# Kernel optimization log

Measured on AMD Instinct MI355X. Metric: run time of the kernel, lower is better.

Reference implementation:

```python
import jax, jax.numpy as jnp
import numpy as np

B, S, ENC = 64, 2048, 1024          # batch, encoder seq len, encoder feature dim
U, E_DIM, V_SZ = 512, 256, 50000    # dec_units, embedding_dim, vocab_size
IN_DIM = ENC + E_DIM                # LSTM input: [context ; token embedding]


def setup_inputs() -> dict:
    key = jax.random.key(0)
    ks = jax.random.split(key, 16)
    g = lambda k, shp, s=0.02: (jax.random.normal(k, shp, jnp.float32) * s)
    return {
        "x": jax.random.randint(ks[0], (B, 1), 0, V_SZ),
        "c_fwd": g(ks[1], (B, U), 0.1),
        "c_bwd": g(ks[2], (B, U), 0.1),
        "enc_output": jax.random.normal(ks[3], (B, S, ENC), jnp.float32),
        "emb": g(ks[4], (V_SZ, E_DIM)),
        "W1_w": g(ks[5], (ENC, U)), "W1_b": jnp.zeros((U,), jnp.float32),
        "W2_w": g(ks[6], (U, U)),   "W2_b": jnp.zeros((U,), jnp.float32),
        "W3_w": g(ks[7], (U, U)),   "W3_b": jnp.zeros((U,), jnp.float32),
        "V_w": g(ks[8], (U, 1)),    "V_b": jnp.zeros((1,), jnp.float32),
        "Kf": g(ks[9], (IN_DIM, 4 * U)),  "bf": jnp.zeros((4 * U,), jnp.float32),
        "Kb": g(ks[10], (IN_DIM, 4 * U)), "bb": jnp.zeros((4 * U,), jnp.float32),
        "fc_w": g(ks[11], (2 * U, V_SZ)), "fc_b": jnp.zeros((V_SZ,), jnp.float32),
    }


def _lstm_step_zero_state(xin, K, b):
    # Keras LSTM single step from zero (h0, c0): recurrent term vanishes.
    # Gate order in Keras kernel: i, f, c(g), o.
    z = xin @ K + b
    i, f, g, o = jnp.split(z, 4, axis=-1)
    i, o = jax.nn.sigmoid(i), jax.nn.sigmoid(o)  # f gate multiplies c0=0
    c = i * jnp.tanh(g)
    h = o * jnp.tanh(c)
    return h, c


def reference(x, c_fwd, c_bwd, enc_output, emb,
              W1_w, W1_b, W2_w, W2_b, W3_w, W3_b, V_w, V_b,
              Kf, bf, Kb, bb, fc_w, fc_b):
    # Bahdanau additive attention: score [B, S, 1]
    hidden_proj = (c_fwd @ W2_w + W2_b + c_bwd @ W3_w + W3_b)[:, None, :]  # [B,1,U]
    score = jnp.tanh(enc_output @ W1_w + W1_b + hidden_proj) @ V_w + V_b
    attn = jax.nn.softmax(score, axis=1)                 # softmax over S
    ctx = jnp.sum(attn * enc_output, axis=1)             # [B, ENC]

    xe = emb[x[:, 0]]                                    # [B, E_DIM]
    xin = jnp.concatenate([ctx, xe], axis=-1)            # [B, ENC+E_DIM]

    # Bidirectional LSTM over a length-1 sequence from zero initial state:
    # both directions see the same single timestep with separate weights.
    hf, cf = _lstm_step_zero_state(xin, Kf, bf)
    hb, cb = _lstm_step_zero_state(xin, Kb, bb)

    out = jnp.concatenate([hf, hb], axis=-1)             # [B, 2U]
    logits = out @ fc_w + fc_b                           # [B, vocab]
    return logits, hf, cf, hb, cb
```

## Files before the change

kernel.cpp:

```cpp
#include <hip/hip_runtime.h>

using u16 = unsigned short;
typedef float f32x4 __attribute__((ext_vector_type(4)));
typedef __bf16 bf16x8 __attribute__((ext_vector_type(8)));
typedef u16 u16x8 __attribute__((ext_vector_type(8)));
typedef u16 u16x4 __attribute__((ext_vector_type(4)));

static constexpr int OF_HPB   = 262144;
static constexpr int OF_CTXP  = 294912;
static constexpr int OF_STATS = 2392064;
static constexpr int OF_XIN   = 2394112;
static constexpr int OF_ZPART = 2476032;
static constexpr size_t SCRATCH_FLOATS = 3000320;
static constexpr size_t SCRATCH_BYTES = SCRATCH_FLOATS * 4ull;

__device__ __forceinline__ u16 f2bf(float f) {
  unsigned u = __float_as_uint(f);
  u += 0x7FFFu + ((u >> 16) & 1u);
  return (u16)(u >> 16);
}
__device__ __forceinline__ float fast_tanh(float x) {
  x = fminf(fmaxf(x, -20.f), 20.f);
  float e = __expf(2.f * x);
  return (e - 1.f) / (e + 1.f);
}
__device__ __forceinline__ float fast_sig(float x) { return 1.f / (1.f + __expf(-x)); }

__device__ __forceinline__ void gll16(const u16* g, u16* l) {
  __builtin_amdgcn_global_load_lds(
      (const __attribute__((address_space(1))) unsigned int*)g,
      (__attribute__((address_space(3))) unsigned int*)l, 16, 0, 0);
}

__global__ void k_prep_w1(const float* __restrict__ W1w, u16* __restrict__ w1p) {
  __shared__ float tile[32][132];
  const int t = threadIdx.x;
  const int ks = blockIdx.x >> 2, u0 = (blockIdx.x & 3) * 128;
  {
    int kk = t >> 3, ui = (t & 7) * 16;
    const float* src = W1w + (size_t)(ks * 32 + kk) * 512 + u0 + ui;
    #pragma unroll
    for (int i = 0; i < 4; ++i)
      *(float4*)&tile[kk][ui + i * 4] = *(const float4*)(src + i * 4);
  }
  __syncthreads();
  {
    int u = t >> 1, kh = (t & 1) * 16;
    u16x8 p0, p1;
    #pragma unroll
    for (int i = 0; i < 8; ++i) {
      p0[i] = f2bf(tile[kh + i][u]);
      p1[i] = f2bf(tile[kh + 8 + i][u]);
    }
    u16* dst = w1p + ((size_t)ks * 512 + u0 + u) * 32 + kh;
    *(u16x8*)(dst)     = p0;
    *(u16x8*)(dst + 8) = p1;
  }
}

__global__ void k_prep_hp(const float* __restrict__ cf, const float* __restrict__ cb,
                          const float* __restrict__ W2w, const float* __restrict__ W2b,
                          const float* __restrict__ W3w, const float* __restrict__ W3b,
                          const float* __restrict__ W1b, float* __restrict__ hpb) {
  __shared__ float cfl[512], cbl[512];
  const int b = blockIdx.x, t = threadIdx.x;
  cfl[t] = cf[(size_t)b * 512 + t];       cfl[t + 256] = cf[(size_t)b * 512 + t + 256];
  cbl[t] = cb[(size_t)b * 512 + t];       cbl[t + 256] = cb[(size_t)b * 512 + t + 256];
  __syncthreads();
  const int u1 = t, u2 = t + 256;
  float a1 = W2b[u1] + W3b[u1] + W1b[u1];
  float a2 = W2b[u2] + W3b[u2] + W1b[u2];
  for (int k = 0; k < 512; ++k) {
    float c1 = cfl[k], c2 = cbl[k];
    const float* r2 = W2w + (size_t)k * 512;
    const float* r3 = W3w + (size_t)k * 512;
    a1 += c1 * r2[u1] + c2 * r3[u1];
    a2 += c1 * r2[u2] + c2 * r3[u2];
  }
  hpb[(size_t)b * 512 + u1] = a1;
  hpb[(size_t)b * 512 + u2] = a2;
}

__global__ void __launch_bounds__(512, 4)
k_attn(const float* __restrict__ enc, const u16* __restrict__ w1p,
       const float* __restrict__ hpb, const float* __restrict__ Vw,
       const float* __restrict__ Vb, float* __restrict__ ctxp,
       float* __restrict__ stats) {
  __shared__ __align__(16) u16 smem[40960];

  const int t = threadIdx.x;
  const int bid = blockIdx.x;
  const int b = bid >> 5, tile = bid & 31;
  const size_t row0 = (size_t)b * 2048 + (size_t)tile * 64;

  const int l = t & 63, w = t >> 6;
  const int ln = l & 15, lg = l >> 4;

  const int s_lg = (t >> 1) & 3, s_ln = (t >> 3) & 15, s_im = t >> 7, s_h = t & 1;
  const float* a_src = enc + (row0 + s_im * 16 + s_ln) * 1024 + s_lg * 8 + s_h * 4;

  f32x4 acc[4][4];
  #pragma unroll
  for (int im = 0; im < 4; ++im)
    #pragma unroll
    for (int nf = 0; nf < 4; ++nf)
      acc[im][nf] = f32x4{0.f, 0.f, 0.f, 0.f};

  {
    u16* Bn = smem;
    #pragma unroll
    for (int i = 0; i < 4; ++i)
      gll16(w1p + i * 4096 + t * 8, Bn + i * 4096 + w * 512);
    float4 av = *(const float4*)(a_src);
    u16x4 aw4;
    aw4[0] = f2bf(av.x); aw4[1] = f2bf(av.y); aw4[2] = f2bf(av.z); aw4[3] = f2bf(av.w);
    *(u16x4*)(smem + 32768 + t * 4) = aw4;
  }
  __syncthreads();

  for (int ks = 0; ks < 32; ++ks) {
    const int cur = ks & 1;
    u16* Bc = smem + cur * 16384;
    u16* Ac = smem + 32768 + cur * 4096;
    float4 av;
    if (ks < 31) {
      u16* Bn = smem + (cur ^ 1) * 16384;
      const u16* bsrc = w1p + (size_t)(ks + 1) * 16384 + t * 8;
      #pragma unroll
      for (int i = 0; i < 4; ++i)
        gll16(bsrc + i * 4096, Bn + i * 4096 + w * 512);
      av = *(const float4*)(a_src + (ks + 1) * 32);
    }
    bf16x8 afr[4], bfr[4];
    #pragma unroll
    for (int im = 0; im < 4; ++im)
      afr[im] = *(const bf16x8*)(Ac + im * 512 + ln * 32 + lg * 8);
    #pragma unroll
    for (int nf = 0; nf < 4; ++nf)
      bfr[nf] = *(const bf16x8*)(Bc + (w * 64 + nf * 16 + ln) * 32 + lg * 8);
    #pragma unroll
    for (int im = 0; im < 4; ++im)
      #pragma unroll
      for (int nf = 0; nf < 4; ++nf)
        acc[im][nf] = __builtin_amdgcn_mfma_f32_16x16x32_bf16(afr[im], bfr[nf], acc[im][nf], 0, 0, 0);
    if (ks < 31) {
      u16* An = smem + 32768 + (cur ^ 1) * 4096;
      u16x4 aw4;
      aw4[0] = f2bf(av.x); aw4[1] = f2bf(av.y); aw4[2] = f2bf(av.z); aw4[3] = f2bf(av.w);
      *(u16x4*)(An + t * 4) = aw4;
    }
    __syncthreads();
  }

  float* fsm = (float*)smem;
  float* red = fsm;
  float* scv = fsm + 576;
  float* pcv = fsm + 640;

  float vw_l[4], hp_l[4];
  #pragma unroll
  for (int nf = 0; nf < 4; ++nf) {
    int col = w * 64 + nf * 16 + ln;
    vw_l[nf] = Vw[col];
    hp_l[nf] = hpb[(size_t)b * 512 + col];
  }
  #pragma unroll
  for (int im = 0; im < 4; ++im) {
    #pragma unroll
    for (int r = 0; r < 4; ++r) {
      float s = 0.f;
      #pragma unroll
      for (int nf = 0; nf < 4; ++nf)
        s += vw_l[nf] * fast_tanh(acc[im][nf][r] + hp_l[nf]);
      s += __shfl_xor(s, 1);
      s += __shfl_xor(s, 2);
      s += __shfl_xor(s, 4);
      s += __shfl_xor(s, 8);
      if (ln == 0) red[(im * 16 + lg * 4 + r) * 9 + w] = s;
    }
  }
  __syncthreads();
  if (t < 64) {
    float s = Vb[0];
    #pragma unroll
    for (int w2 = 0; w2 < 8; ++w2) s += red[t * 9 + w2];
    float e = __expf(s);
    scv[t] = e;
    float p = e;
    p += __shfl_xor(p, 1);  p += __shfl_xor(p, 2);  p += __shfl_xor(p, 4);
    p += __shfl_xor(p, 8);  p += __shfl_xor(p, 16); p += __shfl_xor(p, 32);
    if (t == 0) stats[bid] = p;
  }
  __syncthreads();

  {
    const int c4 = (t & 255) * 4;
    const int rh = t >> 8;
    const float* ep = enc + (row0 + rh * 32) * 1024 + c4;
    float ax = 0.f, ay = 0.f, az = 0.f, aw2 = 0.f;
    #pragma unroll 4
    for (int r = 0; r < 32; ++r) {
      float4 v = *(const float4*)(ep + (size_t)r * 1024);
      float s = scv[rh * 32 + r];
      ax += s * v.x; ay += s * v.y; az += s * v.z; aw2 += s * v.w;
    }
    if (t >= 256) {
      float4 st = {ax, ay, az, aw2};
      *(float4*)&pcv[c4] = st;
    }
    __syncthreads();
    if (t < 256) {
      float4 p2 = *(const float4*)&pcv[c4];
      float4 o = {ax + p2.x, ay + p2.y, az + p2.z, aw2 + p2.w};
      *(float4*)&ctxp[(size_t)bid * 1024 + c4] = o;
    }
  }
}

__global__ void k_attn_reduce(const float* __restrict__ ctxp, const float* __restrict__ stats,
                              const int* __restrict__ x, const float* __restrict__ emb,
                              float* __restrict__ xin) {
  __shared__ float ps[32];
  __shared__ float invs;
  const int b = blockIdx.x, t = threadIdx.x;
  if (t < 32) ps[t] = stats[b * 32 + t];
  __syncthreads();
  if (t == 0) {
    float s = 0.f;
    #pragma unroll
    for (int i = 0; i < 32; ++i) s += ps[i];
    invs = 1.f / s;
  }
  __syncthreads();
  const float inv = invs;
  #pragma unroll
  for (int i = 0; i < 4; ++i) {
    int c = t + i * 256;
    float a = 0.f;
    for (int chv = 0; chv < 32; ++chv)
      a += ctxp[((size_t)b * 32 + chv) * 1024 + c];
    xin[(size_t)b * 1280 + c] = a * inv;
  }
  xin[(size_t)b * 1280 + 1024 + t] = emb[(size_t)x[b] * 256 + t];
}

__global__ void k_lstm_gemm(const float* __restrict__ xin, const float* __restrict__ Kf,
                            const float* __restrict__ Kb, float* __restrict__ zpart) {
  __shared__ float xl[32][68];
  const int t = threadIdx.x;
  const int bid = blockIdx.x;
  const int dir = bid >> 7;
  const int jt  = (bid >> 1) & 63;
  const int ks  = bid & 1;
  const float* K = dir ? Kb : Kf;
  const int j  = jt * 32 + (t & 31);
  const int tb = t >> 5;
  const int brow = t >> 2, kq = (t & 3) * 8;
  float acc[8] = {0,0,0,0,0,0,0,0};
  for (int k0 = ks * 640; k0 < ks * 640 + 640; k0 += 32) {
    float4 x0 = *(const float4*)&xin[(size_t)brow * 1280 + k0 + kq];
    float4 x1 = *(const float4*)&xin[(size_t)brow * 1280 + k0 + kq + 4];
    __syncthreads();
    xl[kq+0][brow]=x0.x; xl[kq+1][brow]=x0.y; xl[kq+2][brow]=x0.z; xl[kq+3][brow]=x0.w;
    xl[kq+4][brow]=x1.x; xl[kq+5][brow]=x1.y; xl[kq+6][brow]=x1.z; xl[kq+7][brow]=x1.w;
    __syncthreads();
    const float* Kp = K + (size_t)k0 * 2048 + j;
    #pragma unroll 8
    for (int kk = 0; kk < 32; ++kk) {
      float wv = Kp[(size_t)kk * 2048];
      float4 v0 = *(const float4*)&xl[kk][tb * 8];
      float4 v1 = *(const float4*)&xl[kk][tb * 8 + 4];
      acc[0] += v0.x * wv; acc[1] += v0.y * wv; acc[2] += v0.z * wv; acc[3] += v0.w * wv;
      acc[4] += v1.x * wv; acc[5] += v1.y * wv; acc[6] += v1.z * wv; acc[7] += v1.w * wv;
    }
  }
  float* zp = zpart + ((size_t)dir * 2 + ks) * 64 * 2048;
  #pragma unroll
  for (int i = 0; i < 8; ++i)
    zp[(size_t)(tb * 8 + i) * 2048 + j] = acc[i];
}

__global__ void k_gates(const float* __restrict__ zpart, const float* __restrict__ bfv,
                        const float* __restrict__ bbv, float* __restrict__ dout) {
  const int dir = blockIdx.x >> 6, b = blockIdx.x & 63, u = threadIdx.x;
  const float* bias = dir ? bbv : bfv;
  const float* z0 = zpart + ((size_t)dir * 2 + 0) * 131072 + (size_t)b * 2048;
  const float* z1 = zpart + ((size_t)dir * 2 + 1) * 131072 + (size_t)b * 2048;
  float zi = z0[u]        + z1[u]        + bias[u];
  float zg = z0[1024 + u] + z1[1024 + u] + bias[1024 + u];
  float zo = z0[1536 + u] + z1[1536 + u] + bias[1536 + u];
  float c = fast_sig(zi) * fast_tanh(zg);
  float h = fast_sig(zo) * fast_tanh(c);
  size_t base = 3200000u + (size_t)dir * 65536u;
  dout[base + (size_t)b * 512 + u] = h;
  dout[base + 32768u + (size_t)b * 512 + u] = c;
}

__global__ void __launch_bounds__(256)
k_fc(const float* __restrict__ dout_ro, const float* __restrict__ fcw,
     const float* __restrict__ fcb, float* __restrict__ logits) {
  __shared__ float ol[64][68];
  __shared__ float wl[64][132];
  const int t = threadIdx.x;
  const int j0 = blockIdx.x * 128;
  const int tb = t >> 5, tj = t & 31;
  const float* hf = dout_ro + 3200000u;
  const float* hb = dout_ro + 3200000u + 65536u;
  float acc[8][4];
  #pragma unroll
  for (int bi = 0; bi < 8; ++bi)
    #pragma unroll
    for (int ji = 0; ji < 4; ++ji) acc[bi][ji] = 0.f;

  for (int k0 = 0; k0 < 1024; k0 += 64) {
    __syncthreads();
    {
      int bb = t >> 2, kq = (t & 3) * 16;
      const float* src = (k0 < 512) ? (hf + (size_t)bb * 512 + k0 + kq)
                                    : (hb + (size_t)bb * 512 + (k0 - 512) + kq);
      #pragma unroll
      for (int i = 0; i < 4; ++i) {
        float4 v = *(const float4*)(src + i * 4);
        ol[kq + i*4 + 0][bb] = v.x;
        ol[kq + i*4 + 1][bb] = v.y;
        ol[kq + i*4 + 2][bb] = v.z;
        ol[kq + i*4 + 3][bb] = v.w;
      }
    }
    {
      int kk = t >> 2, jh = (t & 3) * 32;
      const float* wsrc = fcw + (size_t)(k0 + kk) * 50000 + j0 + jh;
      #pragma unroll
      for (int i = 0; i < 8; ++i) {
        int j = j0 + jh + i * 4;
        float4 v;
        if (j + 3 < 50000) {
          v = *(const float4*)(wsrc + i * 4);
        } else {
          v.x = (j + 0 < 50000) ? wsrc[i*4 + 0] : 0.f;
          v.y = (j + 1 < 50000) ? wsrc[i*4 + 1] : 0.f;
          v.z = (j + 2 < 50000) ? wsrc[i*4 + 2] : 0.f;
          v.w = 0.f;
        }
        *(float4*)&wl[kk][jh + i * 4] = v;
      }
    }
    __syncthreads();
    #pragma unroll 4
    for (int kk = 0; kk < 64; ++kk) {
      float4 wv = *(const float4*)&wl[kk][tj * 4];
      float4 q0 = *(const float4*)&ol[kk][tb * 8];
      float4 q1 = *(const float4*)&ol[kk][tb * 8 + 4];
      float obv[8] = {q0.x, q0.y, q0.z, q0.w, q1.x, q1.y, q1.z, q1.w};
      #pragma unroll
      for (int bi = 0; bi < 8; ++bi) {
        acc[bi][0] += obv[bi] * wv.x;
        acc[bi][1] += obv[bi] * wv.y;
        acc[bi][2] += obv[bi] * wv.z;
        acc[bi][3] += obv[bi] * wv.w;
      }
    }
  }

  const int j = j0 + tj * 4;
  if (j + 3 < 50000) {
    float4 fb = *(const float4*)(fcb + j);
    #pragma unroll
    for (int bi = 0; bi < 8; ++bi) {
      float4 r;
      r.x = acc[bi][0] + fb.x; r.y = acc[bi][1] + fb.y;
      r.z = acc[bi][2] + fb.z; r.w = acc[bi][3] + fb.w;
      *(float4*)&logits[(size_t)(tb * 8 + bi) * 50000 + j] = r;
    }
  } else {
    for (int ji = 0; ji < 4; ++ji) {
      if (j + ji < 50000) {
        float fb = fcb[j + ji];
        for (int bi = 0; bi < 8; ++bi)
          logits[(size_t)(tb * 8 + bi) * 50000 + j + ji] = acc[bi][ji] + fb;
      }
    }
  }
}

extern "C" void kernel_launch(void* const* d_in, const int* in_sizes, int n_in,
                              void* d_out, int out_size, void* d_ws, size_t ws_size,
                              hipStream_t stream) {
  const int*   x    = (const int*)  d_in[0];
  const float* cfwd = (const float*)d_in[1];
  const float* cbwd = (const float*)d_in[2];
  const float* enc  = (const float*)d_in[3];
  const float* emb  = (const float*)d_in[4];
  const float* W1w  = (const float*)d_in[5];
  const float* W1b  = (const float*)d_in[6];
  const float* W2w  = (const float*)d_in[7];
  const float* W2b  = (const float*)d_in[8];
  const float* W3w  = (const float*)d_in[9];
  const float* W3b  = (const float*)d_in[10];
  const float* Vw   = (const float*)d_in[11];
  const float* Vb   = (const float*)d_in[12];
  const float* Kf   = (const float*)d_in[13];
  const float* bfv  = (const float*)d_in[14];
  const float* Kb   = (const float*)d_in[15];
  const float* bbv  = (const float*)d_in[16];
  const float* fcw  = (const float*)d_in[17];
  const float* fcb  = (const float*)d_in[18];
  float* out = (float*)d_out;

  float* S = (ws_size >= SCRATCH_BYTES) ? (float*)d_ws : out;
  u16*   w1p   = (u16*)S;
  float* hpb   = S + OF_HPB;
  float* ctxp  = S + OF_CTXP;
  float* stats = S + OF_STATS;
  float* xin   = S + OF_XIN;
  float* zpart = S + OF_ZPART;

  k_prep_w1<<<128, 256, 0, stream>>>(W1w, w1p);
  k_prep_hp<<<64, 256, 0, stream>>>(cfwd, cbwd, W2w, W2b, W3w, W3b, W1b, hpb);
  k_attn<<<2048, 512, 0, stream>>>(enc, w1p, hpb, Vw, Vb, ctxp, stats);
  k_attn_reduce<<<64, 256, 0, stream>>>(ctxp, stats, x, emb, xin);
  k_lstm_gemm<<<256, 256, 0, stream>>>(xin, Kf, Kb, zpart);
  k_gates<<<128, 512, 0, stream>>>(zpart, bfv, bbv, out);
  k_fc<<<391, 256, 0, stream>>>(out, fcw, fcb, out);
}
```

Baseline: 541.6 us.

## Use bf16 MFMA for vocab projection and deepen attention GEMM prefetch pipeline

Adds a per-call pre-pass that converts fc_w to bf16 in a K-blocked layout, plus an MFMA-based vocab projection that splits the activations into bf16 hi and lo parts to keep fp32-like accuracy. This replaces the fp32 SIMT GEMM whenever the workspace is large enough. The attention GEMM gets a 3-deep register prefetch of encoder rows, relaid LDS fragments, explicit vmcnt waits with raw barriers, and setprio around the MFMA block, all to hide global load latency. The fc weight conversion reads the 200MB fp32 matrix and writes 100MB of bf16 on every call, which may cost more than the faster GEMM saves. The new path also depends on the workspace size.

```diff
diff --git a/kernel.cpp b/kernel.cpp
--- a/kernel.cpp
+++ b/kernel.cpp
@@ -12,12 +12,23 @@
 static constexpr int OF_XIN   = 2394112;
 static constexpr int OF_ZPART = 2476032;
 static constexpr size_t SCRATCH_FLOATS = 3000320;
-static constexpr size_t SCRATCH_BYTES = SCRATCH_FLOATS * 4ull;
+static constexpr size_t SCRATCH_BYTES  = SCRATCH_FLOATS * 4ull;
+static constexpr size_t OF_W2P_F       = 3000320;
+static constexpr size_t W2P_U16        = 50176ull * 1024ull;
+static constexpr size_t TOTAL_BYTES    = OF_W2P_F * 4ull + W2P_U16 * 2ull;
+
+#define FENCE()  asm volatile("" ::: "memory")
+#define VMCNT6() asm volatile("s_waitcnt vmcnt(6)" ::: "memory")
+#define VMCNT0() asm volatile("s_waitcnt vmcnt(0)" ::: "memory")
+#define LGKM0()  asm volatile("s_waitcnt lgkmcnt(0)" ::: "memory")
 
 __device__ __forceinline__ u16 f2bf(float f) {
   unsigned u = __float_as_uint(f);
   u += 0x7FFFu + ((u >> 16) & 1u);
   return (u16)(u >> 16);
+}
+__device__ __forceinline__ float bf2f(u16 u) {
+  return __uint_as_float((unsigned)u << 16);
 }
 __device__ __forceinline__ float fast_tanh(float x) {
   x = fminf(fmaxf(x, -20.f), 20.f);
@@ -81,12 +92,49 @@
   hpb[(size_t)b * 512 + u2] = a2;
 }
 
+__global__ void __launch_bounds__(256)
+k_prep_fcw(const float* __restrict__ fcw, u16* __restrict__ w2p) {
+  __shared__ float tl[32][260];
+  const int t = threadIdx.x;
+  const int jt = blockIdx.x >> 5, kt = blockIdx.x & 31;
+  const int j0 = jt * 256, k0 = kt * 32;
+  {
+    const int kk = t >> 3, c0 = (t & 7) * 32;
+    const float* src = fcw + (size_t)(k0 + kk) * 50000 + j0 + c0;
+    #pragma unroll
+    for (int i = 0; i < 8; ++i) {
+      int j = j0 + c0 + i * 4;
+      float4 v;
+      if (j + 3 < 50000) {
+        v = *(const float4*)(src + i * 4);
+      } else {
+        v.x = (j + 0 < 50000) ? src[i * 4 + 0] : 0.f;
+        v.y = (j + 1 < 50000) ? src[i * 4 + 1] : 0.f;
+        v.z = (j + 2 < 50000) ? src[i * 4 + 2] : 0.f;
+        v.w = 0.f;
+      }
+      *(float4*)&tl[kk][c0 + i * 4] = v;
+    }
+  }
+  __syncthreads();
+  {
+    u16* dst = w2p + ((size_t)kt * 50176 + j0 + t) * 32;
+    #pragma unroll
+    for (int q = 0; q < 4; ++q) {
+      u16x8 p;
+      #pragma unroll
+      for (int m = 0; m < 8; ++m) p[m] = f2bf(tl[q * 8 + m][t]);
+      *(u16x8*)(dst + q * 8) = p;
+    }
+  }
+}
+
 __global__ void __launch_bounds__(512, 4)
 k_attn(const float* __restrict__ enc, const u16* __restrict__ w1p,
        const float* __restrict__ hpb, const float* __restrict__ Vw,
        const float* __restrict__ Vb, float* __restrict__ ctxp,
        float* __restrict__ stats) {
-  __shared__ __align__(16) u16 smem[40960];
+  __shared__ __align__(16) u16 smem[36864];
 
   const int t = threadIdx.x;
   const int bid = blockIdx.x;
@@ -96,60 +144,107 @@
   const int l = t & 63, w = t >> 6;
   const int ln = l & 15, lg = l >> 4;
 
-  const int s_lg = (t >> 1) & 3, s_ln = (t >> 3) & 15, s_im = t >> 7, s_h = t & 1;
+  const int s_im = t >> 7, s_ln = (t >> 3) & 15, s_lg = (t >> 1) & 3, s_h = t & 1;
   const float* a_src = enc + (row0 + s_im * 16 + s_ln) * 1024 + s_lg * 8 + s_h * 4;
+  const int a_dst = (s_im * 64 + s_lg * 16 + s_ln) * 8 + s_h * 4;
+  const u16* bsrc = w1p + (size_t)(w * 64 + ln) * 32 + lg * 8;
+  u16* bdst = smem + w * 2048;
 
   f32x4 acc[4][4];
   #pragma unroll
   for (int im = 0; im < 4; ++im)
     #pragma unroll
-    for (int nf = 0; nf < 4; ++nf)
-      acc[im][nf] = f32x4{0.f, 0.f, 0.f, 0.f};
-
+    for (int nf = 0; nf < 4; ++nf) acc[im][nf] = f32x4{0.f, 0.f, 0.f, 0.f};
+
+  float4 avH0, avH1, avH2;
   {
-    u16* Bn = smem;
-    #pragma unroll
-    for (int i = 0; i < 4; ++i)
-      gll16(w1p + i * 4096 + t * 8, Bn + i * 4096 + w * 512);
-    float4 av = *(const float4*)(a_src);
-    u16x4 aw4;
-    aw4[0] = f2bf(av.x); aw4[1] = f2bf(av.y); aw4[2] = f2bf(av.z); aw4[3] = f2bf(av.w);
-    *(u16x4*)(smem + 32768 + t * 4) = aw4;
-  }
-  __syncthreads();
-
-  for (int ks = 0; ks < 32; ++ks) {
+    float4 av0 = *(const float4*)(a_src);
+    u16x4 aw;
+    aw[0]=f2bf(av0.x); aw[1]=f2bf(av0.y); aw[2]=f2bf(av0.z); aw[3]=f2bf(av0.w);
+    *(u16x4*)(smem + 32768 + a_dst) = aw;
+    FENCE();
+    avH0 = *(const float4*)(a_src + 32);
+    avH1 = *(const float4*)(a_src + 64);
+    FENCE();
+    gll16(bsrc,        bdst);
+    gll16(bsrc +  512, bdst +  512);
+    gll16(bsrc + 1024, bdst + 1024);
+    gll16(bsrc + 1536, bdst + 1536);
+    FENCE();
+    avH2 = *(const float4*)(a_src + 96);
+    FENCE();
+    LGKM0();
+    __builtin_amdgcn_s_barrier();
+  }
+
+  #pragma unroll 4
+  for (int ks = 0; ks < 28; ++ks) {
     const int cur = ks & 1;
-    u16* Bc = smem + cur * 16384;
-    u16* Ac = smem + 32768 + cur * 4096;
-    float4 av;
+    {
+      u16* bd = bdst + ((cur ^ 1) << 14);
+      const u16* bs = bsrc + (size_t)(ks + 1) * 16384;
+      gll16(bs, bd);               gll16(bs +  512, bd +  512);
+      gll16(bs + 1024, bd + 1024); gll16(bs + 1536, bd + 1536);
+    }
+    FENCE();
+    float4 avIn = *(const float4*)(a_src + (ks + 4) * 32);
+    FENCE();
+    VMCNT6();
+    const u16* Ac = smem + 32768 + (cur << 11);
+    const u16* Bc = smem + (cur << 14) + w * 2048;
+    bf16x8 afr[4], bfr[4];
+    #pragma unroll
+    for (int im = 0; im < 4; ++im) afr[im] = *(const bf16x8*)(Ac + im * 512 + l * 8);
+    #pragma unroll
+    for (int nf = 0; nf < 4; ++nf) bfr[nf] = *(const bf16x8*)(Bc + nf * 512 + l * 8);
+    __builtin_amdgcn_s_setprio(1);
+    #pragma unroll
+    for (int im = 0; im < 4; ++im)
+      #pragma unroll
+      for (int nf = 0; nf < 4; ++nf)
+        acc[im][nf] = __builtin_amdgcn_mfma_f32_16x16x32_bf16(afr[im], bfr[nf], acc[im][nf], 0, 0, 0);
+    __builtin_amdgcn_s_setprio(0);
+    {
+      u16* An = smem + 32768 + ((cur ^ 1) << 11);
+      u16x4 aw;
+      aw[0]=f2bf(avH0.x); aw[1]=f2bf(avH0.y); aw[2]=f2bf(avH0.z); aw[3]=f2bf(avH0.w);
+      *(u16x4*)(An + a_dst) = aw;
+    }
+    avH0 = avH1; avH1 = avH2; avH2 = avIn;
+    LGKM0();
+    __builtin_amdgcn_s_barrier();
+  }
+
+  for (int ks = 28; ks < 32; ++ks) {
+    const int cur = ks & 1;
     if (ks < 31) {
-      u16* Bn = smem + (cur ^ 1) * 16384;
-      const u16* bsrc = w1p + (size_t)(ks + 1) * 16384 + t * 8;
-      #pragma unroll
-      for (int i = 0; i < 4; ++i)
-        gll16(bsrc + i * 4096, Bn + i * 4096 + w * 512);
-      av = *(const float4*)(a_src + (ks + 1) * 32);
-    }
+      u16* bd = bdst + ((cur ^ 1) << 14);
+      const u16* bs = bsrc + (size_t)(ks + 1) * 16384;
+      gll16(bs, bd);               gll16(bs +  512, bd +  512);
+      gll16(bs + 1024, bd + 1024); gll16(bs + 1536, bd + 1536);
+    }
+    VMCNT0();
+    const u16* Ac = smem + 32768 + (cur << 11);
+    const u16* Bc = smem + (cur << 14) + w * 2048;
     bf16x8 afr[4], bfr[4];
     #pragma unroll
-    for (int im = 0; im < 4; ++im)
-      afr[im] = *(const bf16x8*)(Ac + im * 512 + ln * 32 + lg * 8);
-    #pragma unroll
-    for (int nf = 0; nf < 4; ++nf)
-      bfr[nf] = *(const bf16x8*)(Bc + (w * 64 + nf * 16 + ln) * 32 + lg * 8);
+    for (int im = 0; im < 4; ++im) afr[im] = *(const bf16x8*)(Ac + im * 512 + l * 8);
+    #pragma unroll
+    for (int nf = 0; nf < 4; ++nf) bfr[nf] = *(const bf16x8*)(Bc + nf * 512 + l * 8);
     #pragma unroll
     for (int im = 0; im < 4; ++im)
       #pragma unroll
       for (int nf = 0; nf < 4; ++nf)
         acc[im][nf] = __builtin_amdgcn_mfma_f32_16x16x32_bf16(afr[im], bfr[nf], acc[im][nf], 0, 0, 0);
     if (ks < 31) {
-      u16* An = smem + 32768 + (cur ^ 1) * 4096;
-      u16x4 aw4;
-      aw4[0] = f2bf(av.x); aw4[1] = f2bf(av.y); aw4[2] = f2bf(av.z); aw4[3] = f2bf(av.w);
-      *(u16x4*)(An + t * 4) = aw4;
-    }
-    __syncthreads();
+      u16* An = smem + 32768 + ((cur ^ 1) << 11);
+      u16x4 aw;
+      aw[0]=f2bf(avH0.x); aw[1]=f2bf(avH0.y); aw[2]=f2bf(avH0.z); aw[3]=f2bf(avH0.w);
+      *(u16x4*)(An + a_dst) = aw;
+      avH0 = avH1; avH1 = avH2;
+    }
+    LGKM0();
+    __builtin_amdgcn_s_barrier();
   }
 
   float* fsm = (float*)smem;
@@ -297,8 +392,117 @@
 }
 
 __global__ void __launch_bounds__(256)
-k_fc(const float* __restrict__ dout_ro, const float* __restrict__ fcw,
-     const float* __restrict__ fcb, float* __restrict__ logits) {
+k_fc_mfma(const float* __restrict__ hbase, const u16* __restrict__ w2p,
+          const float* __restrict__ fcb, float* __restrict__ logits) {
+  __shared__ __align__(16) u16 smem[24576];
+  const int t = threadIdx.x;
+  const int j0 = blockIdx.x * 256;
+  const int l = t & 63, w = t >> 6;
+  const int ln = l & 15, lg = l >> 4;
+
+  const int s_im = t >> 6, s_ln = (t >> 2) & 15, s_lg = t & 3;
+  const int a_chunk = (s_im * 64 + s_lg * 16 + s_ln) * 8;
+  const int a_row = s_im * 16 + s_ln;
+
+  const u16* bsrc = w2p + (size_t)(j0 + w * 64 + ln) * 32 + lg * 8;
+  u16* bdst = smem + w * 2048;
+
+  f32x4 acc[4][4];
+  #pragma unroll
+  for (int im = 0; im < 4; ++im)
+    #pragma unroll
+    for (int nf = 0; nf < 4; ++nf) acc[im][nf] = f32x4{0.f, 0.f, 0.f, 0.f};
+
+  {
+    gll16(bsrc,        bdst);
+    gll16(bsrc +  512, bdst +  512);
+    gll16(bsrc + 1024, bdst + 1024);
+    gll16(bsrc + 1536, bdst + 1536);
+    const float* hs = hbase + (size_t)a_row * 512 + s_lg * 8;
+    float4 v0 = *(const float4*)(hs);
+    float4 v1 = *(const float4*)(hs + 4);
+    float vv[8] = {v0.x, v0.y, v0.z, v0.w, v1.x, v1.y, v1.z, v1.w};
+    u16x8 hi, lo;
+    #pragma unroll
+    for (int jq = 0; jq < 8; ++jq) {
+      u16 h = f2bf(vv[jq]);
+      hi[jq] = h;
+      lo[jq] = f2bf(vv[jq] - bf2f(h));
+    }
+    *(u16x8*)(smem + 16384 + a_chunk) = hi;
+    *(u16x8*)(smem + 16384 + 2048 + a_chunk) = lo;
+  }
+  __syncthreads();
+
+  for (int ks = 0; ks < 32; ++ks) {
+    const int cur = ks & 1;
+    if (ks < 31) {
+      u16* bd = bdst + ((cur ^ 1) << 13);
+      const u16* bs = bsrc + (size_t)(ks + 1) * 1605632;
+      gll16(bs, bd);               gll16(bs +  512, bd +  512);
+      gll16(bs + 1024, bd + 1024); gll16(bs + 1536, bd + 1536);
+    }
+    const u16* Ac = smem + 16384 + (cur << 12);
+    const u16* Bc = smem + (cur << 13) + w * 2048;
+    bf16x8 ahi[4], alo[4], bfr[4];
+    #pragma unroll
+    for (int im = 0; im < 4; ++im) {
+      ahi[im] = *(const bf16x8*)(Ac + im * 512 + l * 8);
+      alo[im] = *(const bf16x8*)(Ac + 2048 + im * 512 + l * 8);
+    }
+    #pragma unroll
+    for (int nf = 0; nf < 4; ++nf) bfr[nf] = *(const bf16x8*)(Bc + nf * 512 + l * 8);
+    #pragma unroll
+    for (int im = 0; im < 4; ++im)
+      #pragma unroll
+      for (int nf = 0; nf < 4; ++nf) {
+        acc[im][nf] = __builtin_amdgcn_mfma_f32_16x16x32_bf16(alo[im], bfr[nf], acc[im][nf], 0, 0, 0);
+        acc[im][nf] = __builtin_amdgcn_mfma_f32_16x16x32_bf16(ahi[im], bfr[nf], acc[im][nf], 0, 0, 0);
+      }
+    if (ks < 31) {
+      const int kn = ks + 1;
+      const float* hs = hbase + (kn >= 16 ? 65536 : 0) + (size_t)a_row * 512 + (kn & 15) * 32 + s_lg * 8;
+      float4 v0 = *(const float4*)(hs);
+      float4 v1 = *(const float4*)(hs + 4);
+      float vv[8] = {v0.x, v0.y, v0.z, v0.w, v1.x, v1.y, v1.z, v1.w};
+      u16x8 hi, lo;
+      #pragma unroll
+      for (int jq = 0; jq < 8; ++jq) {
+        u16 h = f2bf(vv[jq]);
+        hi[jq] = h;
+        lo[jq] = f2bf(vv[jq] - bf2f(h));
+      }
+      u16* An = smem + 16384 + ((cur ^ 1) << 12);
+      *(u16x8*)(An + a_chunk) = hi;
+      *(u16x8*)(An + 2048 + a_chunk) = lo;
+    }
+    __syncthreads();
+  }
+
+  float fb[4];
+  #pragma unroll
+  for (int nf = 0; nf < 4; ++nf) {
+    int c = j0 + w * 64 + nf * 16 + ln;
+    fb[nf] = (c < 50000) ? fcb[c] : 0.f;
+  }
+  #pragma unroll
+  for (int im = 0; im < 4; ++im)
+    #pragma unroll
+    for (int nf = 0; nf < 4; ++nf) {
+      int c = j0 + w * 64 + nf * 16 + ln;
+      if (c < 50000) {
+        #pragma unroll
+        for (int r = 0; r < 4; ++r) {
+          int row = im * 16 + lg * 4 + r;
+          logits[(size_t)row * 50000 + c] = acc[im][nf][r] + fb[nf];
+        }
+      }
+    }
+}
+
+__global__ void __launch_bounds__(256)
+k_fc_f32(const float* __restrict__ dout_ro, const float* __restrict__ fcw,
+         const float* __restrict__ fcb, float* __restrict__ logits) {
   __shared__ float ol[64][68];
   __shared__ float wl[64][132];
   const int t = threadIdx.x;
@@ -407,19 +611,24 @@
   const float* fcb  = (const float*)d_in[18];
   float* out = (float*)d_out;
 
-  float* S = (ws_size >= SCRATCH_BYTES) ? (float*)d_ws : out;
+  const bool haveWs  = (ws_size >= SCRATCH_BYTES);
+  const bool bigWs   = (ws_size >= TOTAL_BYTES);
+  float* S = haveWs ? (float*)d_ws : out;
   u16*   w1p   = (u16*)S;
   float* hpb   = S + OF_HPB;
   float* ctxp  = S + OF_CTXP;
   float* stats = S + OF_STATS;
   float* xin   = S + OF_XIN;
   float* zpart = S + OF_ZPART;
+  u16*   w2p   = (u16*)(S + OF_W2P_F);
 
   k_prep_w1<<<128, 256, 0, stream>>>(W1w, w1p);
   k_prep_hp<<<64, 256, 0, stream>>>(cfwd, cbwd, W2w, W2b, W3w, W3b, W1b, hpb);
+  if (bigWs) k_prep_fcw<<<6272, 256, 0, stream>>>(fcw, w2p);
   k_attn<<<2048, 512, 0, stream>>>(enc, w1p, hpb, Vw, Vb, ctxp, stats);
   k_attn_reduce<<<64, 256, 0, stream>>>(ctxp, stats, x, emb, xin);
   k_lstm_gemm<<<256, 256, 0, stream>>>(xin, Kf, Kb, zpart);
   k_gates<<<128, 512, 0, stream>>>(zpart, bfv, bbv, out);
-  k_fc<<<391, 256, 0, stream>>>(out, fcw, fcb, out);
-}
+  if (bigWs) k_fc_mfma<<<196, 256, 0, stream>>>(out + 3200000u, w2p, fcb, out);
+  else       k_fc_f32<<<391, 256, 0, stream>>>(out, fcw, fcb, out);
+}
```

Result: slower. 591.1 us (+9.1%).

## Move vocab projection to bf16 MFMA with split-precision activations and relayout attention LDS

Applied to the files above, without the earlier changes.

The final FC GEMM (64x1024 by 1024x50000) moves from a scalar fp32 kernel to an MFMA kernel. Hidden states are split into bf16 hi/lo parts by the gates kernel, and fc weights are rounded to bf16 on the fly from a double-buffered LDS tile. The attention GEMM also changes its LDS layout so fragments are read contiguously, uses a smaller shared buffer, and prefetches the encoder rows one step further ahead. The trade-off is reduced weight precision, since the weights go to bf16 while only the activations keep hi/lo compensation, plus a fallback path when the workspace is too small.

```diff
diff --git a/kernel.cpp b/kernel.cpp
--- a/kernel.cpp
+++ b/kernel.cpp
@@ -11,13 +11,17 @@
 static constexpr int OF_STATS = 2392064;
 static constexpr int OF_XIN   = 2394112;
 static constexpr int OF_ZPART = 2476032;
-static constexpr size_t SCRATCH_FLOATS = 3000320;
-static constexpr size_t SCRATCH_BYTES = SCRATCH_FLOATS * 4ull;
+static constexpr int OF_HHL   = 3000320;
+static constexpr size_t SCRATCH_FLOATS = 3065856;
+static constexpr size_t SCRATCH_BYTES  = SCRATCH_FLOATS * 4ull;
 
 __device__ __forceinline__ u16 f2bf(float f) {
   unsigned u = __float_as_uint(f);
   u += 0x7FFFu + ((u >> 16) & 1u);
   return (u16)(u >> 16);
+}
+__device__ __forceinline__ float bf2f(u16 u) {
+  return __uint_as_float((unsigned)u << 16);
 }
 __device__ __forceinline__ float fast_tanh(float x) {
   x = fminf(fmaxf(x, -20.f), 20.f);
@@ -86,7 +90,7 @@
        const float* __restrict__ hpb, const float* __restrict__ Vw,
        const float* __restrict__ Vb, float* __restrict__ ctxp,
        float* __restrict__ stats) {
-  __shared__ __align__(16) u16 smem[40960];
+  __shared__ __align__(16) u16 smem[36864];
 
   const int t = threadIdx.x;
   const int bid = blockIdx.x;
@@ -96,59 +100,57 @@
   const int l = t & 63, w = t >> 6;
   const int ln = l & 15, lg = l >> 4;
 
-  const int s_lg = (t >> 1) & 3, s_ln = (t >> 3) & 15, s_im = t >> 7, s_h = t & 1;
+  const int s_im = t >> 7, s_ln = (t >> 3) & 15, s_lg = (t >> 1) & 3, s_h = t & 1;
   const float* a_src = enc + (row0 + s_im * 16 + s_ln) * 1024 + s_lg * 8 + s_h * 4;
+  const int a_dst = (s_im * 64 + s_lg * 16 + s_ln) * 8 + s_h * 4;
+  const u16* bsrc = w1p + (size_t)(w * 64 + ln) * 32 + lg * 8;
+  u16* bdst = smem + w * 2048;
 
   f32x4 acc[4][4];
   #pragma unroll
   for (int im = 0; im < 4; ++im)
     #pragma unroll
-    for (int nf = 0; nf < 4; ++nf)
-      acc[im][nf] = f32x4{0.f, 0.f, 0.f, 0.f};
-
+    for (int nf = 0; nf < 4; ++nf) acc[im][nf] = f32x4{0.f, 0.f, 0.f, 0.f};
+
+  float4 avB;
   {
-    u16* Bn = smem;
-    #pragma unroll
-    for (int i = 0; i < 4; ++i)
-      gll16(w1p + i * 4096 + t * 8, Bn + i * 4096 + w * 512);
-    float4 av = *(const float4*)(a_src);
-    u16x4 aw4;
-    aw4[0] = f2bf(av.x); aw4[1] = f2bf(av.y); aw4[2] = f2bf(av.z); aw4[3] = f2bf(av.w);
-    *(u16x4*)(smem + 32768 + t * 4) = aw4;
+    float4 av0 = *(const float4*)(a_src);
+    u16x4 aw;
+    aw[0]=f2bf(av0.x); aw[1]=f2bf(av0.y); aw[2]=f2bf(av0.z); aw[3]=f2bf(av0.w);
+    *(u16x4*)(smem + 32768 + a_dst) = aw;
+    gll16(bsrc,        bdst);
+    gll16(bsrc +  512, bdst +  512);
+    gll16(bsrc + 1024, bdst + 1024);
+    gll16(bsrc + 1536, bdst + 1536);
+    avB = *(const float4*)(a_src + 32);
   }
   __syncthreads();
 
   for (int ks = 0; ks < 32; ++ks) {
     const int cur = ks & 1;
-    u16* Bc = smem + cur * 16384;
-    u16* Ac = smem + 32768 + cur * 4096;
-    float4 av;
     if (ks < 31) {
-      u16* Bn = smem + (cur ^ 1) * 16384;
-      const u16* bsrc = w1p + (size_t)(ks + 1) * 16384 + t * 8;
-      #pragma unroll
-      for (int i = 0; i < 4; ++i)
-        gll16(bsrc + i * 4096, Bn + i * 4096 + w * 512);
-      av = *(const float4*)(a_src + (ks + 1) * 32);
-    }
+      u16* An = smem + 32768 + ((cur ^ 1) << 11);
+      u16x4 aw;
+      aw[0]=f2bf(avB.x); aw[1]=f2bf(avB.y); aw[2]=f2bf(avB.z); aw[3]=f2bf(avB.w);
+      *(u16x4*)(An + a_dst) = aw;
+      if (ks < 30) avB = *(const float4*)(a_src + (ks + 2) * 32);
+      u16* bd = bdst + ((cur ^ 1) << 14);
+      const u16* bs = bsrc + (size_t)(ks + 1) * 16384;
+      gll16(bs, bd);               gll16(bs +  512, bd +  512);
+      gll16(bs + 1024, bd + 1024); gll16(bs + 1536, bd + 1536);
+    }
+    const u16* Ac = smem + 32768 + (cur << 11);
+    const u16* Bc = smem + (cur << 14) + w * 2048;
     bf16x8 afr[4], bfr[4];
     #pragma unroll
-    for (int im = 0; im < 4; ++im)
-      afr[im] = *(const bf16x8*)(Ac + im * 512 + ln * 32 + lg * 8);
-    #pragma unroll
-    for (int nf = 0; nf < 4; ++nf)
-      bfr[nf] = *(const bf16x8*)(Bc + (w * 64 + nf * 16 + ln) * 32 + lg * 8);
+    for (int im = 0; im < 4; ++im) afr[im] = *(const bf16x8*)(Ac + im * 512 + l * 8);
+    #pragma unroll
+    for (int nf = 0; nf < 4; ++nf) bfr[nf] = *(const bf16x8*)(Bc + nf * 512 + l * 8);
     #pragma unroll
     for (int im = 0; im < 4; ++im)
       #pragma unroll
       for (int nf = 0; nf < 4; ++nf)
         acc[im][nf] = __builtin_amdgcn_mfma_f32_16x16x32_bf16(afr[im], bfr[nf], acc[im][nf], 0, 0, 0);
-    if (ks < 31) {
-      u16* An = smem + 32768 + (cur ^ 1) * 4096;
-      u16x4 aw4;
-      aw4[0] = f2bf(av.x); aw4[1] = f2bf(av.y); aw4[2] = f2bf(av.z); aw4[3] = f2bf(av.w);
-      *(u16x4*)(An + t * 4) = aw4;
-    }
     __syncthreads();
   }
 
@@ -281,7 +283,8 @@
 }
 
 __global__ void k_gates(const float* __restrict__ zpart, const float* __restrict__ bfv,
-                        const float* __restrict__ bbv, float* __restrict__ dout) {
+                        const float* __restrict__ bbv, float* __restrict__ dout,
+                        u16* __restrict__ hhl) {
   const int dir = blockIdx.x >> 6, b = blockIdx.x & 63, u = threadIdx.x;
   const float* bias = dir ? bbv : bfv;
   const float* z0 = zpart + ((size_t)dir * 2 + 0) * 131072 + (size_t)b * 2048;
@@ -294,11 +297,119 @@
   size_t base = 3200000u + (size_t)dir * 65536u;
   dout[base + (size_t)b * 512 + u] = h;
   dout[base + 32768u + (size_t)b * 512 + u] = c;
+  u16 hi = f2bf(h);
+  u16 lo = f2bf(h - bf2f(hi));
+  hhl[(size_t)b * 1024 + dir * 512 + u] = hi;
+  hhl[65536u + (size_t)b * 1024 + dir * 512 + u] = lo;
 }
 
 __global__ void __launch_bounds__(256)
-k_fc(const float* __restrict__ dout_ro, const float* __restrict__ fcw,
-     const float* __restrict__ fcb, float* __restrict__ logits) {
+k_fc_mfma(const float* __restrict__ fcw, const u16* __restrict__ hhl,
+          const float* __restrict__ fcb, float* __restrict__ logits) {
+  __shared__ float Bs[2][32 * 136];
+  const int t = threadIdx.x;
+  const int j0 = blockIdx.x * 128;
+  const int l = t & 63, w = t >> 6;
+  const int ln = l & 15, lg = l >> 4;
+  const int srow = t >> 3, scol = (t & 7) * 16;
+  const bool interior = (j0 + 128 <= 50000);
+
+  f32x4 acc[4][2];
+  #pragma unroll
+  for (int im = 0; im < 4; ++im)
+    #pragma unroll
+    for (int nf = 0; nf < 2; ++nf) acc[im][nf] = f32x4{0.f, 0.f, 0.f, 0.f};
+
+  float4 pre[4];
+  {
+    const float* src = fcw + (size_t)srow * 50000 + j0 + scol;
+    if (interior) {
+      #pragma unroll
+      for (int q = 0; q < 4; ++q) pre[q] = *(const float4*)(src + q * 4);
+    } else {
+      #pragma unroll
+      for (int q = 0; q < 4; ++q) {
+        int jb = j0 + scol + q * 4;
+        pre[q].x = (jb + 0 < 50000) ? src[q*4 + 0] : 0.f;
+        pre[q].y = (jb + 1 < 50000) ? src[q*4 + 1] : 0.f;
+        pre[q].z = (jb + 2 < 50000) ? src[q*4 + 2] : 0.f;
+        pre[q].w = (jb + 3 < 50000) ? src[q*4 + 3] : 0.f;
+      }
+    }
+    #pragma unroll
+    for (int q = 0; q < 4; ++q)
+      *(float4*)&Bs[0][srow * 136 + scol + q * 4] = pre[q];
+  }
+  __syncthreads();
+
+  for (int ks = 0; ks < 32; ++ks) {
+    const int cur = ks & 1;
+    if (ks < 31) {
+      const float* src = fcw + (size_t)(ks + 1) * 32 * 50000 + (size_t)srow * 50000 + j0 + scol;
+      if (interior) {
+        #pragma unroll
+        for (int q = 0; q < 4; ++q) pre[q] = *(const float4*)(src + q * 4);
+      } else {
+        #pragma unroll
+        for (int q = 0; q < 4; ++q) {
+          int jb = j0 + scol + q * 4;
+          pre[q].x = (jb + 0 < 50000) ? src[q*4 + 0] : 0.f;
+          pre[q].y = (jb + 1 < 50000) ? src[q*4 + 1] : 0.f;
+          pre[q].z = (jb + 2 < 50000) ? src[q*4 + 2] : 0.f;
+          pre[q].w = (jb + 3 < 50000) ? src[q*4 + 3] : 0.f;
+        }
+      }
+    }
+    bf16x8 ahi[4], alo[4];
+    #pragma unroll
+    for (int im = 0; im < 4; ++im) {
+      const u16* ha = hhl + (size_t)(im * 16 + ln) * 1024 + ks * 32 + lg * 8;
+      ahi[im] = *(const bf16x8*)(ha);
+      alo[im] = *(const bf16x8*)(ha + 65536);
+    }
+    bf16x8 bfr[2];
+    #pragma unroll
+    for (int nf = 0; nf < 2; ++nf) {
+      u16x8 pv;
+      #pragma unroll
+      for (int i = 0; i < 8; ++i)
+        pv[i] = f2bf(Bs[cur][(lg * 8 + i) * 136 + w * 32 + nf * 16 + ln]);
+      bfr[nf] = *(bf16x8*)&pv;
+    }
+    #pragma unroll
+    for (int im = 0; im < 4; ++im)
+      #pragma unroll
+      for (int nf = 0; nf < 2; ++nf) {
+        acc[im][nf] = __builtin_amdgcn_mfma_f32_16x16x32_bf16(alo[im], bfr[nf], acc[im][nf], 0, 0, 0);
+        acc[im][nf] = __builtin_amdgcn_mfma_f32_16x16x32_bf16(ahi[im], bfr[nf], acc[im][nf], 0, 0, 0);
+      }
+    if (ks < 31) {
+      #pragma unroll
+      for (int q = 0; q < 4; ++q)
+        *(float4*)&Bs[cur ^ 1][srow * 136 + scol + q * 4] = pre[q];
+    }
+    __syncthreads();
+  }
+
+  #pragma unroll
+  for (int nf = 0; nf < 2; ++nf) {
+    int c = j0 + w * 32 + nf * 16 + ln;
+    if (c < 50000) {
+      float fb = fcb[c];
+      #pragma unroll
+      for (int im = 0; im < 4; ++im)
+        #pragma unroll
+        for (int r = 0; r < 4; ++r) {
+          int row = im * 16 + lg * 4 + r;
+          logits[(size_t)row * 50000 + c] = acc[im][nf][r] + fb;
+        }
+    }
+  }
+}
+
+__global__ void __launch_bounds__(256)
+k_fc_f32(const float* __restrict__ dout_ro, const float* __restrict__ fcw,
+         const float* __restrict__ fcb, float* __restrict__ logits) {
   __shared__ float ol[64][68];
   __shared__ float wl[64][132];
   const int t = threadIdx.x;
@@ -407,19 +518,22 @@
   const float* fcb  = (const float*)d_in[18];
   float* out = (float*)d_out;
 
-  float* S = (ws_size >= SCRATCH_BYTES) ? (float*)d_ws : out;
+  const bool haveWs = (ws_size >= SCRATCH_BYTES);
+  float* S = haveWs ? (float*)d_ws : out;
   u16*   w1p   = (u16*)S;
   float* hpb   = S + OF_HPB;
   float* ctxp  = S + OF_CTXP;
   float* stats = S + OF_STATS;
   float* xin   = S + OF_XIN;
   float* zpart = S + OF_ZPART;
+  u16*   hhl   = (u16*)(S + OF_HHL);
 
   k_prep_w1<<<128, 256, 0, stream>>>(W1w, w1p);
   k_prep_hp<<<64, 256, 0, stream>>>(cfwd, cbwd, W2w, W2b, W3w, W3b, W1b, hpb);
   k_attn<<<2048, 512, 0, stream>>>(enc, w1p, hpb, Vw, Vb, ctxp, stats);
   k_attn_reduce<<<64, 256, 0, stream>>>(ctxp, stats, x, emb, xin);
   k_lstm_gemm<<<256, 256, 0, stream>>>(xin, Kf, Kb, zpart);
-  k_gates<<<128, 512, 0, stream>>>(zpart, bfv, bbv, out);
-  k_fc<<<391, 256, 0, stream>>>(out, fcw, fcb, out);
-}
+  k_gates<<<128, 512, 0, stream>>>(zpart, bfv, bbv, out, hhl);
+  if (haveWs) k_fc_mfma<<<392, 256, 0, stream>>>(fcw, hhl, fcb, out);
+  else        k_fc_f32<<<391, 256, 0, stream>>>(out, fcw, fcb, out);
+}
```

Result: faster. 519.7 us (-4.0%).
